# Kernel optimization log

Measured on AMD Instinct MI355X. Metric: run time of the kernel, lower is better.

## Reference

```python
import jax, jax.numpy as jnp
import numpy as np

B, S, E = 4096, 200, 32

def setup_inputs() -> dict:
    key = jax.random.key(0)
    ks = jax.random.split(key, 8)
    scale = 1.0 / np.sqrt(E)
    return {
        "all_memory": jax.random.normal(ks[0], (B, S, E), jnp.float32),
        "last_memory": jax.random.normal(ks[1], (B, E), jnp.float32),
        "average_memory": jax.random.normal(ks[2], (B, E), jnp.float32),
        "mask": jnp.zeros((B, S), dtype=bool),
        "W1": jax.random.normal(ks[3], (E, E), jnp.float32) * scale,
        "b1": jnp.zeros((E,), jnp.float32),
        "W2": jax.random.normal(ks[4], (E, E), jnp.float32) * scale,
        "b2": jnp.zeros((E,), jnp.float32),
        "W3": jax.random.normal(ks[5], (E, E), jnp.float32) * scale,
        "b3": jnp.zeros((E,), jnp.float32),
        "W4": jax.random.normal(ks[6], (E, 1), jnp.float32) * scale,
    }


def reference(all_memory, last_memory, average_memory, mask, W1, b1, W2, b2, W3, b3, W4):
    # all_memory: [B,S,E]; last/average_memory: [B,E]
    # NOTE: source has `if mask is None: masked_fill_`, so with a provided
    # (non-None) mask the masking branch is dead code -> mask unused.
    proj = (jnp.einsum('bse,ef->bsf', all_memory, W1) + b1
            + (last_memory @ W2 + b2)[:, None, :]
            + (average_memory @ W3 + b3)[:, None, :])  # [B,S,E]
    scores = jax.nn.sigmoid(proj) @ W4  # [B,S,1]
    out = jnp.sum(scores * all_memory, axis=1)  # [B,E]
    return out
```

## Files before the change

kernel.cpp:

```cpp
#include <hip/hip_runtime.h>
#include <hip/hip_bf16.h>

#define B_N 4096
#define S_N 200
#define E_N 32

typedef float f32x4 __attribute__((ext_vector_type(4)));
typedef short s16x8 __attribute__((ext_vector_type(8)));

static __device__ __forceinline__ float sigmoidf_fast(float x) {
    return __builtin_amdgcn_rcpf(1.0f + __expf(-x));
}

__global__ __launch_bounds__(256, 4) void attn_pool_kernel(
    const float* __restrict__ am,
    const float* __restrict__ lastm,
    const float* __restrict__ avgm,
    const float* __restrict__ W1,
    const float* __restrict__ b1,
    const float* __restrict__ W2,
    const float* __restrict__ b2,
    const float* __restrict__ W3,
    const float* __restrict__ b3,
    const float* __restrict__ W4,
    float* __restrict__ out)
{
    const int tid  = threadIdx.x;
    const int l    = tid & 63;
    const int wave = tid >> 6;
    const int b    = blockIdx.x * 4 + wave;

    const int lm = l & 15;
    const int lg = l >> 4;
    const int fi = l & 31;
    const int e0 = 8 * lg;

    s16x8 w1A, w1B, w2A, w2B, w3A, w3B;
#pragma unroll
    for (int i = 0; i < 8; i += 2) {
        int e = e0 + i;
        float2 p;
        p = {W1[e * E_N + lm],      W1[(e + 1) * E_N + lm]};
        ((__hip_bfloat162*)&w1A)[i >> 1] = __float22bfloat162_rn(p);
        p = {W1[e * E_N + 16 + lm], W1[(e + 1) * E_N + 16 + lm]};
        ((__hip_bfloat162*)&w1B)[i >> 1] = __float22bfloat162_rn(p);
        p = {W2[e * E_N + lm],      W2[(e + 1) * E_N + lm]};
        ((__hip_bfloat162*)&w2A)[i >> 1] = __float22bfloat162_rn(p);
        p = {W2[e * E_N + 16 + lm], W2[(e + 1) * E_N + 16 + lm]};
        ((__hip_bfloat162*)&w2B)[i >> 1] = __float22bfloat162_rn(p);
        p = {W3[e * E_N + lm],      W3[(e + 1) * E_N + lm]};
        ((__hip_bfloat162*)&w3A)[i >> 1] = __float22bfloat162_rn(p);
        p = {W3[e * E_N + 16 + lm], W3[(e + 1) * E_N + 16 + lm]};
        ((__hip_bfloat162*)&w3B)[i >> 1] = __float22bfloat162_rn(p);
    }

    s16x8 lfrag, vfrag;
    {
        const f32x4* pl = (const f32x4*)(lastm + (size_t)b * E_N + e0);
        const f32x4* pa = (const f32x4*)(avgm  + (size_t)b * E_N + e0);
        f32x4 l0 = pl[0], l1 = pl[1];
        f32x4 a0 = pa[0], a1 = pa[1];
#pragma unroll
        for (int i = 0; i < 4; i += 2) {
            ((__hip_bfloat162*)&lfrag)[i >> 1]       = __float22bfloat162_rn({l0[i], l0[i + 1]});
            ((__hip_bfloat162*)&lfrag)[(i + 4) >> 1] = __float22bfloat162_rn({l1[i], l1[i + 1]});
            ((__hip_bfloat162*)&vfrag)[i >> 1]       = __float22bfloat162_rn({a0[i], a0[i + 1]});
            ((__hip_bfloat162*)&vfrag)[(i + 4) >> 1] = __float22bfloat162_rn({a1[i], a1[i + 1]});
        }
    }

    float bsum = b1[fi] + b2[fi] + b3[fi];
    f32x4 c0, c1, w4A, w4B;
#pragma unroll
    for (int j = 0; j < 4; ++j) {
        c0[j]  = __shfl(bsum, 4 * lg + j);
        c1[j]  = __shfl(bsum, 16 + 4 * lg + j);
        w4A[j] = W4[4 * lg + j];
        w4B[j] = W4[16 + 4 * lg + j];
    }
    c0 = __builtin_amdgcn_mfma_f32_16x16x32_bf16(w2A, lfrag, c0, 0, 0, 0);
    c0 = __builtin_amdgcn_mfma_f32_16x16x32_bf16(w3A, vfrag, c0, 0, 0, 0);
    c1 = __builtin_amdgcn_mfma_f32_16x16x32_bf16(w2B, lfrag, c1, 0, 0, 0);
    c1 = __builtin_amdgcn_mfma_f32_16x16x32_bf16(w3B, vfrag, c1, 0, 0, 0);

    const float* rowbase = am + (size_t)b * S_N * E_N + e0;

    f32x4 bufs[3][2];
#pragma unroll
    for (int t = 0; t < 3; ++t) {
        const f32x4* p = (const f32x4*)(rowbase + (size_t)(t * 16 + lm) * E_N);
        bufs[t][0] = p[0];
        bufs[t][1] = p[1];
    }

    float acc[8];
#pragma unroll
    for (int i = 0; i < 8; ++i) acc[i] = 0.0f;

#pragma unroll
    for (int t = 0; t < 13; ++t) {
        f32x4 v0 = bufs[t % 3][0];
        f32x4 v1 = bufs[t % 3][1];
        if (t == 12 && lm >= 8) {
            v0 = f32x4{0.0f, 0.0f, 0.0f, 0.0f};
            v1 = f32x4{0.0f, 0.0f, 0.0f, 0.0f};
        }

        s16x8 af;
#pragma unroll
        for (int i = 0; i < 4; i += 2) {
            ((__hip_bfloat162*)&af)[i >> 1]       = __float22bfloat162_rn({v0[i], v0[i + 1]});
            ((__hip_bfloat162*)&af)[(i + 4) >> 1] = __float22bfloat162_rn({v1[i], v1[i + 1]});
        }

        f32x4 d0 = __builtin_amdgcn_mfma_f32_16x16x32_bf16(w1A, af, c0, 0, 0, 0);
        f32x4 d1 = __builtin_amdgcn_mfma_f32_16x16x32_bf16(w1B, af, c1, 0, 0, 0);

        float s = 0.0f;
#pragma unroll
        for (int j = 0; j < 4; ++j) {
            s += w4A[j] * sigmoidf_fast(d0[j]);
            s += w4B[j] * sigmoidf_fast(d1[j]);
        }
        s += __shfl_xor(s, 16);
        s += __shfl_xor(s, 32);

#pragma unroll
        for (int i = 0; i < 4; ++i) {
            acc[i]     += s * v0[i];
            acc[4 + i] += s * v1[i];
        }

        if (t + 3 < 13) {
            const int r = (t + 3) * 16 + lm;
            if (r < S_N) {
                const f32x4* p = (const f32x4*)(rowbase + (size_t)r * E_N);
                bufs[t % 3][0] = p[0];
                bufs[t % 3][1] = p[1];
            }
        }
    }

#pragma unroll
    for (int i = 0; i < 8; ++i) {
        acc[i] += __shfl_xor(acc[i], 1);
        acc[i] += __shfl_xor(acc[i], 2);
        acc[i] += __shfl_xor(acc[i], 4);
        acc[i] += __shfl_xor(acc[i], 8);
    }
    if (lm == 0) {
        f32x4 o0, o1;
#pragma unroll
        for (int i = 0; i < 4; ++i) { o0[i] = acc[i]; o1[i] = acc[4 + i]; }
        f32x4* po = (f32x4*)(out + (size_t)b * E_N + e0);
        po[0] = o0;
        po[1] = o1;
    }
}

extern "C" void kernel_launch(void* const* d_in, const int* in_sizes, int n_in,
                              void* d_out, int out_size, void* d_ws, size_t ws_size,
                              hipStream_t stream) {
    const float* am    = (const float*)d_in[0];
    const float* lastm = (const float*)d_in[1];
    const float* avgm  = (const float*)d_in[2];
    const float* W1 = (const float*)d_in[4];
    const float* b1 = (const float*)d_in[5];
    const float* W2 = (const float*)d_in[6];
    const float* b2 = (const float*)d_in[7];
    const float* W3 = (const float*)d_in[8];
    const float* b3 = (const float*)d_in[9];
    const float* W4 = (const float*)d_in[10];
    float* out = (float*)d_out;

    dim3 grid(B_N / 4);
    dim3 block(256);
    hipLaunchKernelGGL(attn_pool_kernel, grid, block, 0, stream,
                       am, lastm, avgm, W1, b1, W2, b2, W3, b3, W4, out);
}
```

Measured before the change: 199.3 us.

## Stream all_memory tiles through LDS with async global_load_lds pipeline

Replaces the register-based triple buffer of all_memory rows with direct global-to-LDS asynchronous loads into a four-slot per-wave LDS ring, gated by explicit vmcnt waits. The intent is to free VGPRs and keep three tiles in flight without register pressure, overlapping memory latency with MFMA and sigmoid work. It adds 32KB of LDS per block, which may limit occupancy, plus LDS read traffic and a dependence on hand-counted waitcnt values. Out-of-range rows are clamped to the last row rather than skipped.

```diff
diff --git a/kernel.cpp b/kernel.cpp
--- a/kernel.cpp
+++ b/kernel.cpp
@@ -8,9 +8,59 @@
 typedef float f32x4 __attribute__((ext_vector_type(4)));
 typedef short s16x8 __attribute__((ext_vector_type(8)));
 
+#define AS1 __attribute__((address_space(1)))
+#define AS3 __attribute__((address_space(3)))
+
 static __device__ __forceinline__ float sigmoidf_fast(float x) {
     return __builtin_amdgcn_rcpf(1.0f + __expf(-x));
 }
+
+#define STAGE(T) do {                                                          \
+    int _row = (T) * 16 + lm;                                                  \
+    if (_row > S_N - 1) _row = S_N - 1;          \
+    const char* _g = amb + (size_t)_row * 128 + lg * 32;                       \
+    char* _l0 = myl + ((T) % 4) * 2048;                                        \
+    __builtin_amdgcn_global_load_lds((const AS1 void*)_g, (AS3 void*)_l0,      \
+                                     16, 0, 0);                                \
+    __builtin_amdgcn_global_load_lds((const AS1 void*)(_g + 16),               \
+                                     (AS3 void*)(_l0 + 1024), 16, 0, 0);       \
+} while (0)
+
+#define WAITV(N) do {                                                          \
+    asm volatile("s_waitcnt vmcnt(" #N ")" ::: "memory");                      \
+    __builtin_amdgcn_sched_barrier(0);                                         \
+} while (0)
+
+#define TILE(T, WN) do {                                                       \
+    if ((T) + 3 < 13) STAGE((T) + 3);                                          \
+    WAITV(WN);                                                                 \
+    f32x4 v0 = *(const f32x4*)(myl + ((T) % 4) * 2048 + l * 16);               \
+    f32x4 v1 = *(const f32x4*)(myl + ((T) % 4) * 2048 + 1024 + l * 16);        \
+    if ((T) == 12 && lm >= 8) {                \
+        v0 = f32x4{0.0f, 0.0f, 0.0f, 0.0f};                                    \
+        v1 = f32x4{0.0f, 0.0f, 0.0f, 0.0f};                                    \
+    }                                                                          \
+    s16x8 af;                                                                  \
+    ((__hip_bfloat162*)&af)[0] = __float22bfloat162_rn({v0[0], v0[1]});        \
+    ((__hip_bfloat162*)&af)[1] = __float22bfloat162_rn({v0[2], v0[3]});        \
+    ((__hip_bfloat162*)&af)[2] = __float22bfloat162_rn({v1[0], v1[1]});        \
+    ((__hip_bfloat162*)&af)[3] = __float22bfloat162_rn({v1[2], v1[3]});        \
+    f32x4 d0 = __builtin_amdgcn_mfma_f32_16x16x32_bf16(w1A, af, c0, 0, 0, 0);  \
+    f32x4 d1 = __builtin_amdgcn_mfma_f32_16x16x32_bf16(w1B, af, c1, 0, 0, 0);  \
+    float s = 0.0f;                                                            \
+    _Pragma("unroll")                                                          \
+    for (int j = 0; j < 4; ++j) {                                              \
+        s += w4A[j] * sigmoidf_fast(d0[j]);                                    \
+        s += w4B[j] * sigmoidf_fast(d1[j]);                                    \
+    }                                                                          \
+    s += __shfl_xor(s, 16);                                                    \
+    s += __shfl_xor(s, 32);                                                    \
+    _Pragma("unroll")                                                          \
+    for (int i = 0; i < 4; ++i) {                                              \
+        acc[i]     += s * v0[i];                                               \
+        acc[4 + i] += s * v1[i];                                               \
+    }                                                                          \
+} while (0)
 
 __global__ __launch_bounds__(256, 4) void attn_pool_kernel(
     const float* __restrict__ am,
@@ -25,6 +75,8 @@
     const float* __restrict__ W4,
     float* __restrict__ out)
 {
+    __shared__ char lds[4][4][2048];
+
     const int tid  = threadIdx.x;
     const int l    = tid & 63;
     const int wave = tid >> 6;
@@ -83,63 +135,18 @@
     c1 = __builtin_amdgcn_mfma_f32_16x16x32_bf16(w2B, lfrag, c1, 0, 0, 0);
     c1 = __builtin_amdgcn_mfma_f32_16x16x32_bf16(w3B, vfrag, c1, 0, 0, 0);
 
-    const float* rowbase = am + (size_t)b * S_N * E_N + e0;
+    const char* amb = (const char*)(am + (size_t)b * S_N * E_N);
+    char* myl = &lds[wave][0][0];
 
-    f32x4 bufs[3][2];
-#pragma unroll
-    for (int t = 0; t < 3; ++t) {
-        const f32x4* p = (const f32x4*)(rowbase + (size_t)(t * 16 + lm) * E_N);
-        bufs[t][0] = p[0];
-        bufs[t][1] = p[1];
-    }
+    STAGE(0); STAGE(1); STAGE(2);
 
     float acc[8];
 #pragma unroll
     for (int i = 0; i < 8; ++i) acc[i] = 0.0f;
 
-#pragma unroll
-    for (int t = 0; t < 13; ++t) {
-        f32x4 v0 = bufs[t % 3][0];
-        f32x4 v1 = bufs[t % 3][1];
-        if (t == 12 && lm >= 8) {
-            v0 = f32x4{0.0f, 0.0f, 0.0f, 0.0f};
-            v1 = f32x4{0.0f, 0.0f, 0.0f, 0.0f};
-        }
-
-        s16x8 af;
-#pragma unroll
-        for (int i = 0; i < 4; i += 2) {
-            ((__hip_bfloat162*)&af)[i >> 1]       = __float22bfloat162_rn({v0[i], v0[i + 1]});
-            ((__hip_bfloat162*)&af)[(i + 4) >> 1] = __float22bfloat162_rn({v1[i], v1[i + 1]});
-        }
-
-        f32x4 d0 = __builtin_amdgcn_mfma_f32_16x16x32_bf16(w1A, af, c0, 0, 0, 0);
-        f32x4 d1 = __builtin_amdgcn_mfma_f32_16x16x32_bf16(w1B, af, c1, 0, 0, 0);
-
-        float s = 0.0f;
-#pragma unroll
-        for (int j = 0; j < 4; ++j) {
-            s += w4A[j] * sigmoidf_fast(d0[j]);
-            s += w4B[j] * sigmoidf_fast(d1[j]);
-        }
-        s += __shfl_xor(s, 16);
-        s += __shfl_xor(s, 32);
-
-#pragma unroll
-        for (int i = 0; i < 4; ++i) {
-            acc[i]     += s * v0[i];
-            acc[4 + i] += s * v1[i];
-        }
-
-        if (t + 3 < 13) {
-            const int r = (t + 3) * 16 + lm;
-            if (r < S_N) {
-                const f32x4* p = (const f32x4*)(rowbase + (size_t)r * E_N);
-                bufs[t % 3][0] = p[0];
-                bufs[t % 3][1] = p[1];
-            }
-        }
-    }
+    TILE(0, 6);  TILE(1, 6);  TILE(2, 6);  TILE(3, 6);  TILE(4, 6);
+    TILE(5, 6);  TILE(6, 6);  TILE(7, 6);  TILE(8, 6);  TILE(9, 6);
+    TILE(10, 4); TILE(11, 2); TILE(12, 0);
 
 #pragma unroll
     for (int i = 0; i < 8; ++i) {
```

Measured after the change: 219.8 us. +10.3%, slower.

## Split each batch row's sequence across two waves with shared-memory reduction

Applied to the files above, without the earlier changes.

Each batch element is now processed by two waves, each covering about half of the 200 sequence rows (7 and 6 tiles of 16), and the partial sums are combined through shared memory after a block barrier. The grid doubles to 2048 blocks. The occupancy hint rises to 8 blocks per SIMD and the 3-deep register prefetch becomes a single-tile double buffer, which lowers register pressure. The aim is more waves in flight to hide memory latency on this bandwidth-bound pooling. The cost is duplicated weight and projection setup per wave plus an added barrier and LDS reduction.

```diff
diff --git a/kernel.cpp b/kernel.cpp
--- a/kernel.cpp
+++ b/kernel.cpp
@@ -12,7 +12,7 @@
     return __builtin_amdgcn_rcpf(1.0f + __expf(-x));
 }
 
-__global__ __launch_bounds__(256, 4) void attn_pool_kernel(
+__global__ __launch_bounds__(256, 8) void attn_pool_kernel(
     const float* __restrict__ am,
     const float* __restrict__ lastm,
     const float* __restrict__ avgm,
@@ -25,93 +25,110 @@
     const float* __restrict__ W4,
     float* __restrict__ out)
 {
+    __shared__ float red[2][2][32];
+
     const int tid  = threadIdx.x;
     const int l    = tid & 63;
     const int wave = tid >> 6;
-    const int b    = blockIdx.x * 4 + wave;
+    const int bs   = wave >> 1;
+    const int h    = wave & 1;
+    const int b    = blockIdx.x * 2 + bs;
 
     const int lm = l & 15;
     const int lg = l >> 4;
     const int fi = l & 31;
     const int e0 = 8 * lg;
 
-    s16x8 w1A, w1B, w2A, w2B, w3A, w3B;
-#pragma unroll
-    for (int i = 0; i < 8; i += 2) {
-        int e = e0 + i;
-        float2 p;
-        p = {W1[e * E_N + lm],      W1[(e + 1) * E_N + lm]};
-        ((__hip_bfloat162*)&w1A)[i >> 1] = __float22bfloat162_rn(p);
-        p = {W1[e * E_N + 16 + lm], W1[(e + 1) * E_N + 16 + lm]};
-        ((__hip_bfloat162*)&w1B)[i >> 1] = __float22bfloat162_rn(p);
-        p = {W2[e * E_N + lm],      W2[(e + 1) * E_N + lm]};
-        ((__hip_bfloat162*)&w2A)[i >> 1] = __float22bfloat162_rn(p);
-        p = {W2[e * E_N + 16 + lm], W2[(e + 1) * E_N + 16 + lm]};
-        ((__hip_bfloat162*)&w2B)[i >> 1] = __float22bfloat162_rn(p);
-        p = {W3[e * E_N + lm],      W3[(e + 1) * E_N + lm]};
-        ((__hip_bfloat162*)&w3A)[i >> 1] = __float22bfloat162_rn(p);
-        p = {W3[e * E_N + 16 + lm], W3[(e + 1) * E_N + 16 + lm]};
-        ((__hip_bfloat162*)&w3B)[i >> 1] = __float22bfloat162_rn(p);
-    }
-
-    s16x8 lfrag, vfrag;
+    s16x8 w1A, w1B;
+    f32x4 c0, c1, w4A, w4B;
     {
-        const f32x4* pl = (const f32x4*)(lastm + (size_t)b * E_N + e0);
-        const f32x4* pa = (const f32x4*)(avgm  + (size_t)b * E_N + e0);
-        f32x4 l0 = pl[0], l1 = pl[1];
-        f32x4 a0 = pa[0], a1 = pa[1];
-#pragma unroll
-        for (int i = 0; i < 4; i += 2) {
-            ((__hip_bfloat162*)&lfrag)[i >> 1]       = __float22bfloat162_rn({l0[i], l0[i + 1]});
-            ((__hip_bfloat162*)&lfrag)[(i + 4) >> 1] = __float22bfloat162_rn({l1[i], l1[i + 1]});
-            ((__hip_bfloat162*)&vfrag)[i >> 1]       = __float22bfloat162_rn({a0[i], a0[i + 1]});
-            ((__hip_bfloat162*)&vfrag)[(i + 4) >> 1] = __float22bfloat162_rn({a1[i], a1[i + 1]});
-        }
-    }
-
-    float bsum = b1[fi] + b2[fi] + b3[fi];
-    f32x4 c0, c1, w4A, w4B;
-#pragma unroll
-    for (int j = 0; j < 4; ++j) {
-        c0[j]  = __shfl(bsum, 4 * lg + j);
-        c1[j]  = __shfl(bsum, 16 + 4 * lg + j);
-        w4A[j] = W4[4 * lg + j];
-        w4B[j] = W4[16 + 4 * lg + j];
-    }
-    c0 = __builtin_amdgcn_mfma_f32_16x16x32_bf16(w2A, lfrag, c0, 0, 0, 0);
-    c0 = __builtin_amdgcn_mfma_f32_16x16x32_bf16(w3A, vfrag, c0, 0, 0, 0);
-    c1 = __builtin_amdgcn_mfma_f32_16x16x32_bf16(w2B, lfrag, c1, 0, 0, 0);
-    c1 = __builtin_amdgcn_mfma_f32_16x16x32_bf16(w3B, vfrag, c1, 0, 0, 0);
-
-    const float* rowbase = am + (size_t)b * S_N * E_N + e0;
-
-    f32x4 bufs[3][2];
-#pragma unroll
-    for (int t = 0; t < 3; ++t) {
-        const f32x4* p = (const f32x4*)(rowbase + (size_t)(t * 16 + lm) * E_N);
-        bufs[t][0] = p[0];
-        bufs[t][1] = p[1];
-    }
+        s16x8 w2A, w2B, w3A, w3B;
+#pragma unroll
+        for (int i = 0; i < 8; i += 2) {
+            int e = e0 + i;
+            float2 p;
+            p = {W1[e * E_N + lm],      W1[(e + 1) * E_N + lm]};
+            ((__hip_bfloat162*)&w1A)[i >> 1] = __float22bfloat162_rn(p);
+            p = {W1[e * E_N + 16 + lm], W1[(e + 1) * E_N + 16 + lm]};
+            ((__hip_bfloat162*)&w1B)[i >> 1] = __float22bfloat162_rn(p);
+            p = {W2[e * E_N + lm],      W2[(e + 1) * E_N + lm]};
+            ((__hip_bfloat162*)&w2A)[i >> 1] = __float22bfloat162_rn(p);
+            p = {W2[e * E_N + 16 + lm], W2[(e + 1) * E_N + 16 + lm]};
+            ((__hip_bfloat162*)&w2B)[i >> 1] = __float22bfloat162_rn(p);
+            p = {W3[e * E_N + lm],      W3[(e + 1) * E_N + lm]};
+            ((__hip_bfloat162*)&w3A)[i >> 1] = __float22bfloat162_rn(p);
+            p = {W3[e * E_N + 16 + lm], W3[(e + 1) * E_N + 16 + lm]};
+            ((__hip_bfloat162*)&w3B)[i >> 1] = __float22bfloat162_rn(p);
+        }
+
+        s16x8 lfrag, vfrag;
+        {
+            const f32x4* pl = (const f32x4*)(lastm + (size_t)b * E_N + e0);
+            const f32x4* pa = (const f32x4*)(avgm  + (size_t)b * E_N + e0);
+            f32x4 l0 = pl[0], l1 = pl[1];
+            f32x4 a0 = pa[0], a1 = pa[1];
+#pragma unroll
+            for (int i = 0; i < 4; i += 2) {
+                ((__hip_bfloat162*)&lfrag)[i >> 1]       = __float22bfloat162_rn({l0[i], l0[i + 1]});
+                ((__hip_bfloat162*)&lfrag)[(i + 4) >> 1] = __float22bfloat162_rn({l1[i], l1[i + 1]});
+                ((__hip_bfloat162*)&vfrag)[i >> 1]       = __float22bfloat162_rn({a0[i], a0[i + 1]});
+                ((__hip_bfloat162*)&vfrag)[(i + 4) >> 1] = __float22bfloat162_rn({a1[i], a1[i + 1]});
+            }
+        }
+
+        float bsum = b1[fi] + b2[fi] + b3[fi];
+#pragma unroll
+        for (int j = 0; j < 4; ++j) {
+            c0[j]  = __shfl(bsum, 4 * lg + j);
+            c1[j]  = __shfl(bsum, 16 + 4 * lg + j);
+            w4A[j] = W4[4 * lg + j];
+            w4B[j] = W4[16 + 4 * lg + j];
+        }
+        c0 = __builtin_amdgcn_mfma_f32_16x16x32_bf16(w2A, lfrag, c0, 0, 0, 0);
+        c0 = __builtin_amdgcn_mfma_f32_16x16x32_bf16(w3A, vfrag, c0, 0, 0, 0);
+        c1 = __builtin_amdgcn_mfma_f32_16x16x32_bf16(w2B, lfrag, c1, 0, 0, 0);
+        c1 = __builtin_amdgcn_mfma_f32_16x16x32_bf16(w3B, vfrag, c1, 0, 0, 0);
+    }
+
+    const int row0 = h * 112;
+    const int nt   = 7 - h;
+    const float* rowbase = am + ((size_t)b * S_N + row0) * E_N + e0;
 
     float acc[8];
 #pragma unroll
     for (int i = 0; i < 8; ++i) acc[i] = 0.0f;
 
-#pragma unroll
-    for (int t = 0; t < 13; ++t) {
-        f32x4 v0 = bufs[t % 3][0];
-        f32x4 v1 = bufs[t % 3][1];
-        if (t == 12 && lm >= 8) {
-            v0 = f32x4{0.0f, 0.0f, 0.0f, 0.0f};
-            v1 = f32x4{0.0f, 0.0f, 0.0f, 0.0f};
+    float amf[8], nxt[8];
+    {
+        const f32x4* p = (const f32x4*)(rowbase + (size_t)lm * E_N);
+        f32x4 v0 = p[0], v1 = p[1];
+#pragma unroll
+        for (int i = 0; i < 4; ++i) { amf[i] = v0[i]; amf[4 + i] = v1[i]; }
+    }
+
+    for (int t = 0; t < nt; ++t) {
+        if (t + 1 < nt) {
+            int r = (t + 1) * 16 + lm;
+            if (row0 + r > S_N - 1) r = S_N - 1 - row0;
+            const f32x4* p = (const f32x4*)(rowbase + (size_t)r * E_N);
+            f32x4 v0 = p[0], v1 = p[1];
+#pragma unroll
+            for (int i = 0; i < 4; ++i) { nxt[i] = v0[i]; nxt[4 + i] = v1[i]; }
+        }
+
+        float v0[4], v1[4];
+        const bool dead = (h == 1) && (t == 5) && (lm >= 8);
+#pragma unroll
+        for (int i = 0; i < 4; ++i) {
+            v0[i] = dead ? 0.0f : amf[i];
+            v1[i] = dead ? 0.0f : amf[4 + i];
         }
 
         s16x8 af;
-#pragma unroll
-        for (int i = 0; i < 4; i += 2) {
-            ((__hip_bfloat162*)&af)[i >> 1]       = __float22bfloat162_rn({v0[i], v0[i + 1]});
-            ((__hip_bfloat162*)&af)[(i + 4) >> 1] = __float22bfloat162_rn({v1[i], v1[i + 1]});
-        }
+        ((__hip_bfloat162*)&af)[0] = __float22bfloat162_rn({v0[0], v0[1]});
+        ((__hip_bfloat162*)&af)[1] = __float22bfloat162_rn({v0[2], v0[3]});
+        ((__hip_bfloat162*)&af)[2] = __float22bfloat162_rn({v1[0], v1[1]});
+        ((__hip_bfloat162*)&af)[3] = __float22bfloat162_rn({v1[2], v1[3]});
 
         f32x4 d0 = __builtin_amdgcn_mfma_f32_16x16x32_bf16(w1A, af, c0, 0, 0, 0);
         f32x4 d1 = __builtin_amdgcn_mfma_f32_16x16x32_bf16(w1B, af, c1, 0, 0, 0);
@@ -130,15 +147,8 @@
             acc[i]     += s * v0[i];
             acc[4 + i] += s * v1[i];
         }
-
-        if (t + 3 < 13) {
-            const int r = (t + 3) * 16 + lm;
-            if (r < S_N) {
-                const f32x4* p = (const f32x4*)(rowbase + (size_t)r * E_N);
-                bufs[t % 3][0] = p[0];
-                bufs[t % 3][1] = p[1];
-            }
-        }
+#pragma unroll
+        for (int i = 0; i < 8; ++i) amf[i] = nxt[i];
     }
 
 #pragma unroll
@@ -148,10 +158,21 @@
         acc[i] += __shfl_xor(acc[i], 4);
         acc[i] += __shfl_xor(acc[i], 8);
     }
+
     if (lm == 0) {
         f32x4 o0, o1;
 #pragma unroll
         for (int i = 0; i < 4; ++i) { o0[i] = acc[i]; o1[i] = acc[4 + i]; }
+        *(f32x4*)&red[bs][h][e0]     = o0;
+        *(f32x4*)&red[bs][h][e0 + 4] = o1;
+    }
+    __syncthreads();
+    if (h == 0 && lm == 0) {
+        f32x4 p0 = *(const f32x4*)&red[bs][1][e0];
+        f32x4 p1 = *(const f32x4*)&red[bs][1][e0 + 4];
+        f32x4 o0, o1;
+#pragma unroll
+        for (int i = 0; i < 4; ++i) { o0[i] = acc[i] + p0[i]; o1[i] = acc[4 + i] + p1[i]; }
         f32x4* po = (f32x4*)(out + (size_t)b * E_N + e0);
         po[0] = o0;
         po[1] = o1;
@@ -173,7 +194,7 @@
     const float* W4 = (const float*)d_in[10];
     float* out = (float*)d_out;
 
-    dim3 grid(B_N / 4);
+    dim3 grid(B_N / 2);
     dim3 block(256);
     hipLaunchKernelGGL(attn_pool_kernel, grid, block, 0, stream,
                        am, lastm, avgm, W1, b1, W2, b2, W3, b3, W4, out);
```

Result: faster. 177.4 us (-11.0%).
